# Optimization experiments

Hardware: AMD Instinct MI355X
Metric: run time of the kernel (lower is better)

## Reference

```python
import jax, jax.numpy as jnp
import numpy as np

N_EMBD = 768
N_HEAD = 12
BLOCK_SIZE = 1024


def setup_inputs() -> dict:
    key = jax.random.key(0)
    ks = jax.random.split(key, 11)
    s = lambda fan_in: 1.0 / np.sqrt(fan_in)
    x = jax.random.normal(ks[0], (8, 1024, N_EMBD), dtype=jnp.float32)
    return {
        "x": x,
        "ln1_g": jnp.ones((N_EMBD,), jnp.float32),
        "ln1_b": jnp.zeros((N_EMBD,), jnp.float32),
        "w_attn": jax.random.normal(ks[1], (N_EMBD, 3 * N_EMBD), jnp.float32) * s(N_EMBD),
        "b_attn": jnp.zeros((3 * N_EMBD,), jnp.float32),
        "w_proj": jax.random.normal(ks[2], (N_EMBD, N_EMBD), jnp.float32) * s(N_EMBD),
        "b_proj": jnp.zeros((N_EMBD,), jnp.float32),
        "ln2_g": jnp.ones((N_EMBD,), jnp.float32),
        "ln2_b": jnp.zeros((N_EMBD,), jnp.float32),
        "w_fc": jax.random.normal(ks[3], (N_EMBD, 4 * N_EMBD), jnp.float32) * s(N_EMBD),
        "b_fc": jnp.zeros((4 * N_EMBD,), jnp.float32),
        "w_fc_proj": jax.random.normal(ks[4], (4 * N_EMBD, N_EMBD), jnp.float32) * s(4 * N_EMBD),
        "b_fc_proj": jnp.zeros((N_EMBD,), jnp.float32),
    }


def _layernorm(x, g, b, eps=1e-5):
    mu = jnp.mean(x, axis=-1, keepdims=True)
    var = jnp.var(x, axis=-1, keepdims=True)
    return (x - mu) * jax.lax.rsqrt(var + eps) * g + b


def _gelu_tanh(x):
    # GELU with tanh approximation (matches nn.GELU(approximate='tanh'))
    c = np.sqrt(2.0 / np.pi).astype(np.float32)
    return 0.5 * x * (1.0 + jnp.tanh(c * (x + 0.044715 * x * x * x)))


def _attn(x, w_attn, b_attn, w_proj, b_proj):
    B, T, C = x.shape
    hs = C // N_HEAD
    qkv = x @ w_attn + b_attn  # [B,T,3C]
    q, k, v = jnp.split(qkv, 3, axis=-1)
    # [B,T,C] -> [B,nh,T,hs]
    to_heads = lambda t: t.reshape(B, T, N_HEAD, hs).transpose(0, 2, 1, 3)
    q, k, v = to_heads(q), to_heads(k), to_heads(v)
    att = jnp.einsum('bhqd,bhkd->bhqk', q, k) * (1.0 / np.sqrt(hs))
    causal = jnp.tril(jnp.ones((T, T), bool))
    att = jnp.where(causal, att, -jnp.inf)
    att = jax.nn.softmax(att, axis=-1)
    y = jnp.einsum('bhqk,bhkd->bhqd', att, v)  # [B,nh,T,hs]
    y = y.transpose(0, 2, 1, 3).reshape(B, T, C)
    return y @ w_proj + b_proj


def reference(x, ln1_g, ln1_b, w_attn, b_attn, w_proj, b_proj,
              ln2_g, ln2_b, w_fc, b_fc, w_fc_proj, b_fc_proj):
    x = x + _attn(_layernorm(x, ln1_g, ln1_b), w_attn, b_attn, w_proj, b_proj)
    h = _layernorm(x, ln2_g, ln2_b)
    h = _gelu_tanh(h @ w_fc + b_fc) @ w_fc_proj + b_fc_proj
    return x + h
```

## Files before the change

### kernel.cpp

```cpp
#include <hip/hip_runtime.h>

typedef __bf16 bf16x8 __attribute__((ext_vector_type(8)));
typedef float  f32x4  __attribute__((ext_vector_type(4)));
typedef unsigned short ushort8 __attribute__((ext_vector_type(8)));

__device__ __forceinline__ unsigned short f2bf(float f) {
    unsigned u = __float_as_uint(f);
    u += 0x7FFFu + ((u >> 16) & 1u);
    return (unsigned short)(u >> 16);
}

__device__ __forceinline__ f32x4 mfma16x16x32(bf16x8 a, bf16x8 b, f32x4 c) {
    return __builtin_amdgcn_mfma_f32_16x16x32_bf16(a, b, c, 0, 0, 0);
}

__device__ __forceinline__ bf16x8 ld8(const unsigned short* p) {
    return __builtin_bit_cast(bf16x8, *(const ushort8*)p);
}

__device__ __forceinline__ float exp2_fast(float x) {
    float r; asm("v_exp_f32 %0, %1" : "=v"(r) : "v"(x)); return r;
}

__device__ __forceinline__ void glds16(const unsigned short* g, unsigned short* l) {
    __builtin_amdgcn_global_load_lds(
        (const __attribute__((address_space(1))) void*)g,
        (__attribute__((address_space(3))) void*)l, 16, 0, 0);
}

__device__ __forceinline__ float gelu_tanh(float x) {
    const float c = 0.7978845608028654f;
    float z = c * (x + 0.044715f * x * x * x);
    float e = __expf(2.f * z);
    float th = 1.f - 2.f / (e + 1.f);
    return 0.5f * x * (1.f + th);
}

#define N_EMBD 768
#define SEQ    1024
#define NHEAD  12
#define HS     64
#define MROWS  8192

__global__ __launch_bounds__(256) void tcast_kernel(const float* __restrict__ in,
                                                    unsigned short* __restrict__ out,
                                                    int K, int N) {
    __shared__ float tile[32][33];
    int nb = blockIdx.x * 32, kb = blockIdx.y * 32;
    int tx = threadIdx.x, ty = threadIdx.y;
#pragma unroll
    for (int i = 0; i < 4; i++) {
        int k = kb + ty + i * 8;
        tile[ty + i * 8][tx] = in[(size_t)k * N + nb + tx];
    }
    __syncthreads();
#pragma unroll
    for (int i = 0; i < 4; i++) {
        int n = nb + ty + i * 8;
        out[(size_t)n * K + kb + tx] = f2bf(tile[tx][ty + i * 8]);
    }
}

__global__ __launch_bounds__(256) void ln_kernel(const float* __restrict__ x,
                                                 const float* __restrict__ g,
                                                 const float* __restrict__ b,
                                                 unsigned short* __restrict__ out) {
    const int row = blockIdx.x * 4 + (threadIdx.x >> 6);
    const int lane = threadIdx.x & 63;
    const float* xr = x + (size_t)row * N_EMBD;
    float v[12], s = 0.f, s2 = 0.f;
#pragma unroll
    for (int i = 0; i < 12; i++) {
        v[i] = xr[lane + i * 64];
        s += v[i]; s2 += v[i] * v[i];
    }
#pragma unroll
    for (int m = 1; m < 64; m <<= 1) { s += __shfl_xor(s, m); s2 += __shfl_xor(s2, m); }
    float mu  = s * (1.f / N_EMBD);
    float var = s2 * (1.f / N_EMBD) - mu * mu;
    float inv = rsqrtf(var + 1e-5f);
#pragma unroll
    for (int i = 0; i < 12; i++) {
        int c = lane + i * 64;
        out[(size_t)row * N_EMBD + c] = f2bf((v[i] - mu) * inv * g[c] + b[c]);
    }
}

template <int EPI, int WM>
__global__ __launch_bounds__(256) void gemm_bt_kernel(
    const unsigned short* __restrict__ A, const unsigned short* __restrict__ BT,
    const float* __restrict__ bias, const float* __restrict__ res,
    float* __restrict__ outF, unsigned short* __restrict__ outB,
    int M, int N, int K) {
    constexpr int BM = WM * 32;
    constexpr int ASZ = BM * 64;
    constexpr int BSZ = 128 * 64;
    __shared__ __attribute__((aligned(16))) unsigned short As[2 * ASZ];
    __shared__ __attribute__((aligned(16))) unsigned short Bs[2 * BSZ];
    const int gx = gridDim.x;
    const int slot = blockIdx.y * gx + blockIdx.x;
    const int chunk = (gx * gridDim.y) >> 3;
    const int logical = (slot & 7) * chunk + (slot >> 3);
    const int m0 = (logical / gx) * BM, n0 = (logical % gx) * 128;
    const int t = threadIdx.x, lane = t & 63, wid = t >> 6;
    const int wr = wid >> 1, wc = wid & 1;

    f32x4 acc[WM][4] = {};

    const int rrow = lane & 15, g = lane >> 4;
    const int swz8 = (rrow & 7) << 3;

    const int srow = t >> 3;
    const int scol = ((t & 7) ^ (srow & 7)) * 8;

    const int NT = K >> 6;

    const unsigned short* aP[WM];
    const unsigned short* bP[4];
#pragma unroll
    for (int i = 0; i < WM; i++) aP[i] = &A[(size_t)(m0 + i * 32 + srow) * K + scol];
#pragma unroll
    for (int i = 0; i < 4; i++)  bP[i] = &BT[(size_t)(n0 + i * 32 + srow) * K + scol];

    auto stage = [&](int buf) {
#pragma unroll
        for (int i = 0; i < WM; i++) {
            glds16(aP[i], &As[buf * ASZ + i * 2048 + wid * 512]);
            aP[i] += 64;
        }
#pragma unroll
        for (int i = 0; i < 4; i++) {
            glds16(bP[i], &Bs[buf * BSZ + i * 2048 + wid * 512]);
            bP[i] += 64;
        }
    };

    stage(0);
    __syncthreads();

    int cur = 0;
    for (int kt = 0; kt < NT; ++kt) {
        if (kt + 1 < NT) stage(cur ^ 1);
        const unsigned short* ab = &As[cur * ASZ];
        const unsigned short* bb = &Bs[cur * BSZ];
#pragma unroll
        for (int s = 0; s < 2; s++) {
            bf16x8 af[WM], bfr[4];
#pragma unroll
            for (int i = 0; i < WM; i++) {
                int row = wr * (WM * 16) + i * 16 + rrow;
                af[i] = ld8(&ab[row * 64 + ((((s << 2) | g) << 3) ^ swz8)]);
            }
#pragma unroll
            for (int j = 0; j < 4; j++) {
                int row = wc * 64 + j * 16 + rrow;
                bfr[j] = ld8(&bb[row * 64 + ((((s << 2) | g) << 3) ^ swz8)]);
            }
#pragma unroll
            for (int i = 0; i < WM; i++)
#pragma unroll
                for (int j = 0; j < 4; j++) acc[i][j] = mfma16x16x32(af[i], bfr[j], acc[i][j]);
        }
        __syncthreads();
        cur ^= 1;
    }

    const int crow = g * 4, ccol = rrow;
#pragma unroll
    for (int i = 0; i < WM; i++) {
        int gr0 = m0 + wr * (WM * 16) + i * 16 + crow;
#pragma unroll
        for (int j = 0; j < 4; j++) {
            int gc = n0 + wc * 64 + j * 16 + ccol;
            float bv = bias[gc];
#pragma unroll
            for (int r = 0; r < 4; r++) {
                int gr = gr0 + r;
                float v = acc[i][j][r] + bv;
                if constexpr (EPI == 1) v = gelu_tanh(v);
                if constexpr (EPI == 2) {
                    outF[(size_t)gr * N + gc] = v + res[(size_t)gr * N + gc];
                } else {
                    outB[(size_t)gr * N + gc] = f2bf(v);
                }
            }
        }
    }
}

#define SCALE_LOG2E 0.18033688011112042f

__global__ __launch_bounds__(256, 4) void attn_kernel(const unsigned short* __restrict__ qkv,
                                                      unsigned short* __restrict__ yb) {
    const int slot = blockIdx.y * 8 + blockIdx.x;
    const int logical = (slot & 7) * 96 + (slot >> 3);
    const int p = logical & 7;
    const int bh = logical >> 3;
    const int b = bh / NHEAD, h = bh % NHEAD;
    const int t = threadIdx.x, lane = t & 63, wid = t >> 6;
    const int q0A = p * 64 + wid * 16, q0B = (15 - p) * 64 + wid * 16;
    const int ntA = p + 1, ntB = 16 - p;
    const int rrow = lane & 15, g = lane >> 4, kg8 = g * 8;

    __shared__ __attribute__((aligned(16))) unsigned short Ks[64 * 64];
    __shared__ __attribute__((aligned(16))) unsigned short Vt[64 * 88];
    __shared__ __attribute__((aligned(16))) unsigned short Ps[4][2][16 * 80];

    bf16x8 qfA[2], qfB[2];
    {
        size_t baseA = ((size_t)(b * SEQ + q0A + rrow)) * 2304 + h * HS;
        qfA[0] = ld8(&qkv[baseA + kg8]);
        qfA[1] = ld8(&qkv[baseA + 32 + kg8]);
        size_t baseB = ((size_t)(b * SEQ + q0B + rrow)) * 2304 + h * HS;
        qfB[0] = ld8(&qkv[baseB + kg8]);
        qfB[1] = ld8(&qkv[baseB + 32 + kg8]);
    }

    f32x4 yA[4] = {}, yB[4] = {};
    float lA[4] = {0.f, 0.f, 0.f, 0.f}, lB[4] = {0.f, 0.f, 0.f, 0.f};

    const int kr0 = t >> 3, kr1 = kr0 + 32;
    const int kc0 = ((t & 7) ^ (kr0 & 7)) * 8;
    const int vd = t & 63, vk = (t >> 6) * 16;

    unsigned short* PB = &Ps[wid][0][0];
    unsigned short* PA = &Ps[wid][1][0];
    const bf16x8 vones = __builtin_bit_cast(bf16x8,
        (ushort8){0x3F80, 0x3F80, 0x3F80, 0x3F80, 0x3F80, 0x3F80, 0x3F80, 0x3F80});

    for (int tt = 0; tt < ntB; tt++) {
        const int kv0 = tt * 64;
        const bool doA = (tt < ntA);
        const bool maskB = (tt == ntB - 1), maskA = (tt == ntA - 1);
        __syncthreads();
        glds16(&qkv[((size_t)(b * SEQ + kv0 + kr0)) * 2304 + 768 + h * HS + kc0], &Ks[wid * 512]);
        glds16(&qkv[((size_t)(b * SEQ + kv0 + kr1)) * 2304 + 768 + h * HS + kc0], &Ks[2048 + wid * 512]);
        ushort8 vlo, vhi;
#pragma unroll
        for (int i = 0; i < 8; i++)
            vlo[i] = qkv[((size_t)(b * SEQ + kv0 + vk + i)) * 2304 + 1536 + h * HS + vd];
#pragma unroll
        for (int i = 0; i < 8; i++)
            vhi[i] = qkv[((size_t)(b * SEQ + kv0 + vk + 8 + i)) * 2304 + 1536 + h * HS + vd];
        *(ushort8*)&Vt[vd * 88 + vk] = vlo;
        *(ushort8*)&Vt[vd * 88 + vk + 8] = vhi;
        __syncthreads();

        f32x4 sB[4], sA[4];
#pragma unroll
        for (int ct = 0; ct < 4; ct++) {
            const int j = ct * 16 + rrow;
            const unsigned short* kr = &Ks[j * 64];
            bf16x8 k0 = ld8(&kr[((g    ) ^ (j & 7)) * 8]);
            bf16x8 k1 = ld8(&kr[((g + 4) ^ (j & 7)) * 8]);
            f32x4 zB = {};
            zB = mfma16x16x32(qfB[0], k0, zB);
            zB = mfma16x16x32(qfB[1], k1, zB);
            sB[ct] = zB;
            if (doA) {
                f32x4 zA = {};
                zA = mfma16x16x32(qfA[0], k0, zA);
                zA = mfma16x16x32(qfA[1], k1, zA);
                sA[ct] = zA;
            }
        }
        const int qrbB = q0B + g * 4, qrbA = q0A + g * 4;
#pragma unroll
        for (int ct = 0; ct < 4; ct++) {
            const int j = ct * 16 + rrow, jj = kv0 + j;
#pragma unroll
            for (int r = 0; r < 4; r++) {
                float v = sB[ct][r] * SCALE_LOG2E;
                if (maskB && jj > qrbB + r) v = -1e30f;
                const int q = g * 4 + r;
                PB[q * 80 + (j ^ ((q & 7) << 3))] = f2bf(exp2_fast(v));
            }
        }
        if (doA) {
#pragma unroll
            for (int ct = 0; ct < 4; ct++) {
                const int j = ct * 16 + rrow, jj = kv0 + j;
#pragma unroll
                for (int r = 0; r < 4; r++) {
                    float v = sA[ct][r] * SCALE_LOG2E;
                    if (maskA && jj > qrbA + r) v = -1e30f;
                    const int q = g * 4 + r;
                    PA[q * 80 + (j ^ ((q & 7) << 3))] = f2bf(exp2_fast(v));
                }
            }
        }
        asm volatile("s_waitcnt lgkmcnt(0)" ::: "memory");
        __builtin_amdgcn_sched_barrier(0);
        const int sw = (rrow & 7) << 3;
        bf16x8 paB0 = ld8(&PB[rrow * 80 + ((kg8     ) ^ sw)]);
        bf16x8 paB1 = ld8(&PB[rrow * 80 + ((kg8 + 32) ^ sw)]);
        bf16x8 paA0, paA1;
        if (doA) {
            paA0 = ld8(&PA[rrow * 80 + ((kg8     ) ^ sw)]);
            paA1 = ld8(&PA[rrow * 80 + ((kg8 + 32) ^ sw)]);
        }
        __builtin_amdgcn_s_setprio(1);
        f32x4 ssB = {};
        ssB = mfma16x16x32(paB0, vones, ssB);
        ssB = mfma16x16x32(paB1, vones, ssB);
#pragma unroll
        for (int r = 0; r < 4; r++) lB[r] += ssB[r];
        if (doA) {
            f32x4 ssA = {};
            ssA = mfma16x16x32(paA0, vones, ssA);
            ssA = mfma16x16x32(paA1, vones, ssA);
#pragma unroll
            for (int r = 0; r < 4; r++) lA[r] += ssA[r];
        }
#pragma unroll
        for (int dt = 0; dt < 4; dt++) {
            const unsigned short* vr = &Vt[(dt * 16 + rrow) * 88];
            bf16x8 v0 = ld8(&vr[kg8]);
            bf16x8 v1 = ld8(&vr[kg8 + 32]);
            yB[dt] = mfma16x16x32(paB0, v0, yB[dt]);
            yB[dt] = mfma16x16x32(paB1, v1, yB[dt]);
            if (doA) {
                yA[dt] = mfma16x16x32(paA0, v0, yA[dt]);
                yA[dt] = mfma16x16x32(paA1, v1, yA[dt]);
            }
        }
        __builtin_amdgcn_s_setprio(0);
    }

#pragma unroll
    for (int dt = 0; dt < 4; dt++)
#pragma unroll
        for (int r = 0; r < 4; r++) {
            int col = h * HS + dt * 16 + rrow;
            yb[((size_t)(b * SEQ + q0B + g * 4 + r)) * N_EMBD + col] = f2bf(yB[dt][r] / lB[r]);
            yb[((size_t)(b * SEQ + q0A + g * 4 + r)) * N_EMBD + col] = f2bf(yA[dt][r] / lA[r]);
        }
}

extern "C" void kernel_launch(void* const* d_in, const int* in_sizes, int n_in,
                              void* d_out, int out_size, void* d_ws, size_t ws_size,
                              hipStream_t stream) {
    const float* x        = (const float*)d_in[0];
    const float* ln1_g    = (const float*)d_in[1];
    const float* ln1_b    = (const float*)d_in[2];
    const float* w_attn   = (const float*)d_in[3];
    const float* b_attn   = (const float*)d_in[4];
    const float* w_proj   = (const float*)d_in[5];
    const float* b_proj   = (const float*)d_in[6];
    const float* ln2_g    = (const float*)d_in[7];
    const float* ln2_b    = (const float*)d_in[8];
    const float* w_fc     = (const float*)d_in[9];
    const float* b_fc     = (const float*)d_in[10];
    const float* w_fcp    = (const float*)d_in[11];
    const float* b_fcp    = (const float*)d_in[12];
    float* out = (float*)d_out;

    unsigned short* ws = (unsigned short*)d_ws;
    unsigned short* wT_attn = ws;
    unsigned short* wT_proj = wT_attn + 2304 * 768;
    unsigned short* wT_fc   = wT_proj + 768 * 768;
    unsigned short* wT_fcp  = wT_fc   + 3072 * 768;
    unsigned short* xb      = wT_fcp  + 768 * 3072;
    unsigned short* qkv     = xb      + (size_t)MROWS * 768;
    unsigned short* yb      = qkv     + (size_t)MROWS * 2304;
    unsigned short* act     = qkv;
    float* x2 = (float*)(yb + (size_t)MROWS * 768);

    dim3 tb(32, 8);
    tcast_kernel<<<dim3(2304 / 32, 768 / 32), tb, 0, stream>>>(w_attn, wT_attn, 768, 2304);
    tcast_kernel<<<dim3(768 / 32, 768 / 32),  tb, 0, stream>>>(w_proj, wT_proj, 768, 768);
    tcast_kernel<<<dim3(3072 / 32, 768 / 32), tb, 0, stream>>>(w_fc,   wT_fc,   768, 3072);
    tcast_kernel<<<dim3(768 / 32, 3072 / 32), tb, 0, stream>>>(w_fcp,  wT_fcp,  3072, 768);

    ln_kernel<<<MROWS / 4, 256, 0, stream>>>(x, ln1_g, ln1_b, xb);
    gemm_bt_kernel<0, 4><<<dim3(2304 / 128, MROWS / 128), 256, 0, stream>>>(
        xb, wT_attn, b_attn, nullptr, nullptr, qkv, MROWS, 2304, 768);
    attn_kernel<<<dim3(8, 96), 256, 0, stream>>>(qkv, yb);
    gemm_bt_kernel<2, 2><<<dim3(768 / 128, MROWS / 64), 256, 0, stream>>>(
        yb, wT_proj, b_proj, x, x2, nullptr, MROWS, 768, 768);
    ln_kernel<<<MROWS / 4, 256, 0, stream>>>(x2, ln2_g, ln2_b, xb);
    gemm_bt_kernel<1, 4><<<dim3(3072 / 128, MROWS / 128), 256, 0, stream>>>(
        xb, wT_fc, b_fc, nullptr, nullptr, act, MROWS, 3072, 768);
    gemm_bt_kernel<2, 2><<<dim3(768 / 128, MROWS / 64), 256, 0, stream>>>(
        act, wT_fcp, b_fcp, x2, out, nullptr, MROWS, 768, 3072);
}
```

Baseline: 253.2 us.

## Add two-wave 128x128 GEMM kernel with 64x128 per-wave tiles for large GEMMs

Adds a new GEMM kernel that runs two waves per block, each computing a 64x128 output sub-tile with a 4x8 accumulator array. The goal is more register-level reuse of A and B fragments per LDS read. It replaces the QKV, FC and FC-proj GEMMs; the FC-proj GEMM also moves from 64-row to 128-row tiles, which halves its grid. The cost is a much higher register count (128 accumulator floats per lane), lower occupancy, and fewer blocks for the N=768 GEMM.

```diff
diff --git a/kernel.cpp b/kernel.cpp
--- a/kernel.cpp
+++ b/kernel.cpp
@@ -83,6 +83,92 @@
     for (int i = 0; i < 12; i++) {
         int c = lane + i * 64;
         out[(size_t)row * N_EMBD + c] = f2bf((v[i] - mu) * inv * g[c] + b[c]);
+    }
+}
+
+template <int EPI>
+__global__ __launch_bounds__(128) void gemm_w2_kernel(
+    const unsigned short* __restrict__ A, const unsigned short* __restrict__ BT,
+    const float* __restrict__ bias, const float* __restrict__ res,
+    float* __restrict__ outF, unsigned short* __restrict__ outB,
+    int M, int N, int K) {
+    __shared__ __attribute__((aligned(16))) unsigned short As[2 * 8192];
+    __shared__ __attribute__((aligned(16))) unsigned short Bs[2 * 8192];
+    const int gx = gridDim.x;
+    const int slot = blockIdx.y * gx + blockIdx.x;
+    const int chunk = (gx * gridDim.y) >> 3;
+    const int logical = (slot & 7) * chunk + (slot >> 3);
+    const int m0 = (logical / gx) * 128, n0 = (logical % gx) * 128;
+    const int t = threadIdx.x, lane = t & 63, w = t >> 6;
+    const int rrow = lane & 15, g = lane >> 4;
+    const int swz8 = (rrow & 7) << 3;
+
+    f32x4 acc[4][8] = {};
+
+    const int srow = t >> 3;
+    const int scol = ((t & 7) ^ (srow & 7)) * 8;
+    const unsigned short* aP = &A[(size_t)(m0 + srow) * K + scol];
+    const unsigned short* bP = &BT[(size_t)(n0 + srow) * K + scol];
+    const int dbase = w * 512;
+
+    const int NT = K >> 6;
+
+    auto stage = [&](int buf) {
+#pragma unroll
+        for (int i = 0; i < 8; i++)
+            glds16(aP + (size_t)(i * 16) * K, &As[buf * 8192 + i * 1024 + dbase]);
+#pragma unroll
+        for (int i = 0; i < 8; i++)
+            glds16(bP + (size_t)(i * 16) * K, &Bs[buf * 8192 + i * 1024 + dbase]);
+        aP += 64; bP += 64;
+    };
+
+    stage(0);
+    __syncthreads();
+
+    int cur = 0;
+    for (int kt = 0; kt < NT; ++kt) {
+        if (kt + 1 < NT) stage(cur ^ 1);
+        const unsigned short* ab = &As[cur * 8192];
+        const unsigned short* bb = &Bs[cur * 8192];
+#pragma unroll
+        for (int s = 0; s < 2; s++) {
+            const int ko = (((s << 2) | g) << 3) ^ swz8;
+            bf16x8 af[4];
+#pragma unroll
+            for (int i = 0; i < 4; i++)
+                af[i] = ld8(&ab[(w * 64 + i * 16 + rrow) * 64 + ko]);
+#pragma unroll
+            for (int j = 0; j < 8; j++) {
+                bf16x8 bf = ld8(&bb[(j * 16 + rrow) * 64 + ko]);
+#pragma unroll
+                for (int i = 0; i < 4; i++)
+                    acc[i][j] = mfma16x16x32(af[i], bf, acc[i][j]);
+            }
+        }
+        __syncthreads();
+        cur ^= 1;
+    }
+
+#pragma unroll
+    for (int i = 0; i < 4; i++) {
+        int gr0 = m0 + w * 64 + i * 16 + g * 4;
+#pragma unroll
+        for (int j = 0; j < 8; j++) {
+            int gc = n0 + j * 16 + rrow;
+            float bv = bias[gc];
+#pragma unroll
+            for (int r = 0; r < 4; r++) {
+                int gr = gr0 + r;
+                float v = acc[i][j][r] + bv;
+                if constexpr (EPI == 1) v = gelu_tanh(v);
+                if constexpr (EPI == 2) {
+                    outF[(size_t)gr * N + gc] = v + res[(size_t)gr * N + gc];
+                } else {
+                    outB[(size_t)gr * N + gc] = f2bf(v);
+                }
+            }
+        }
     }
 }
 
@@ -373,14 +459,14 @@
     tcast_kernel<<<dim3(768 / 32, 3072 / 32), tb, 0, stream>>>(w_fcp,  wT_fcp,  3072, 768);
 
     ln_kernel<<<MROWS / 4, 256, 0, stream>>>(x, ln1_g, ln1_b, xb);
-    gemm_bt_kernel<0, 4><<<dim3(2304 / 128, MROWS / 128), 256, 0, stream>>>(
+    gemm_w2_kernel<0><<<dim3(2304 / 128, MROWS / 128), 128, 0, stream>>>(
         xb, wT_attn, b_attn, nullptr, nullptr, qkv, MROWS, 2304, 768);
     attn_kernel<<<dim3(8, 96), 256, 0, stream>>>(qkv, yb);
     gemm_bt_kernel<2, 2><<<dim3(768 / 128, MROWS / 64), 256, 0, stream>>>(
         yb, wT_proj, b_proj, x, x2, nullptr, MROWS, 768, 768);
     ln_kernel<<<MROWS / 4, 256, 0, stream>>>(x2, ln2_g, ln2_b, xb);
-    gemm_bt_kernel<1, 4><<<dim3(3072 / 128, MROWS / 128), 256, 0, stream>>>(
+    gemm_w2_kernel<1><<<dim3(3072 / 128, MROWS / 128), 128, 0, stream>>>(
         xb, wT_fc, b_fc, nullptr, nullptr, act, MROWS, 3072, 768);
-    gemm_bt_kernel<2, 2><<<dim3(768 / 128, MROWS / 64), 256, 0, stream>>>(
+    gemm_w2_kernel<2><<<dim3(768 / 128, MROWS / 128), 128, 0, stream>>>(
         act, wT_fcp, b_fcp, x2, out, nullptr, MROWS, 768, 3072);
 }
```

New measurement: 302.6 us. 1.19x slower.

## Load 128-key KV tiles per barrier pair and share one P buffer

Applied to the files above, without the earlier changes.

The attention kernel now stages 128 keys of K and V into shared memory per iteration and processes them as two 64-key sub-steps, which halves the number of __syncthreads round trips per KV sweep. The B and A query groups are handled one after the other through a single per-wave P scratch buffer instead of two, with occupancy dropped from 4 to 3 blocks per SM to fit the larger LDS footprint. The costs are lower occupancy, serialised A/B softmax phases, and some wasted loading when ntB is odd.

```diff
diff --git a/kernel.cpp b/kernel.cpp
--- a/kernel.cpp
+++ b/kernel.cpp
@@ -190,7 +190,7 @@
 
 #define SCALE_LOG2E 0.18033688011112042f
 
-__global__ __launch_bounds__(256, 4) void attn_kernel(const unsigned short* __restrict__ qkv,
+__global__ __launch_bounds__(256, 3) void attn_kernel(const unsigned short* __restrict__ qkv,
                                                       unsigned short* __restrict__ yb) {
     const int slot = blockIdx.y * 8 + blockIdx.x;
     const int logical = (slot & 7) * 96 + (slot >> 3);
@@ -200,11 +200,12 @@
     const int t = threadIdx.x, lane = t & 63, wid = t >> 6;
     const int q0A = p * 64 + wid * 16, q0B = (15 - p) * 64 + wid * 16;
     const int ntA = p + 1, ntB = 16 - p;
+    const int ntT = (ntB + 1) >> 1;
     const int rrow = lane & 15, g = lane >> 4, kg8 = g * 8;
 
-    __shared__ __attribute__((aligned(16))) unsigned short Ks[64 * 64];
-    __shared__ __attribute__((aligned(16))) unsigned short Vt[64 * 88];
-    __shared__ __attribute__((aligned(16))) unsigned short Ps[4][2][16 * 80];
+    __shared__ __attribute__((aligned(16))) unsigned short Ks[128 * 64];
+    __shared__ __attribute__((aligned(16))) unsigned short Vt[64 * 152];
+    __shared__ __attribute__((aligned(16))) unsigned short Ps[4][16 * 80];
 
     bf16x8 qfA[2], qfB[2];
     {
@@ -219,112 +220,123 @@
     f32x4 yA[4] = {}, yB[4] = {};
     float lA[4] = {0.f, 0.f, 0.f, 0.f}, lB[4] = {0.f, 0.f, 0.f, 0.f};
 
-    const int kr0 = t >> 3, kr1 = kr0 + 32;
-    const int kc0 = ((t & 7) ^ (kr0 & 7)) * 8;
-    const int vd = t & 63, vk = (t >> 6) * 16;
-
-    unsigned short* PB = &Ps[wid][0][0];
-    unsigned short* PA = &Ps[wid][1][0];
+    const int kr = t >> 3;
+    const int kc = ((t & 7) ^ (kr & 7)) * 8;
+    const int vd = t & 63, vk = (t >> 6) * 32;
+
+    unsigned short* P = &Ps[wid][0];
     const bf16x8 vones = __builtin_bit_cast(bf16x8,
         (ushort8){0x3F80, 0x3F80, 0x3F80, 0x3F80, 0x3F80, 0x3F80, 0x3F80, 0x3F80});
-
-    for (int tt = 0; tt < ntB; tt++) {
-        const int kv0 = tt * 64;
-        const bool doA = (tt < ntA);
-        const bool maskB = (tt == ntB - 1), maskA = (tt == ntA - 1);
+    const int sw = (rrow & 7) << 3;
+
+    for (int tt = 0; tt < ntT; tt++) {
+        const int kv0 = tt * 128;
         __syncthreads();
-        glds16(&qkv[((size_t)(b * SEQ + kv0 + kr0)) * 2304 + 768 + h * HS + kc0], &Ks[wid * 512]);
-        glds16(&qkv[((size_t)(b * SEQ + kv0 + kr1)) * 2304 + 768 + h * HS + kc0], &Ks[2048 + wid * 512]);
-        ushort8 vlo, vhi;
-#pragma unroll
-        for (int i = 0; i < 8; i++)
-            vlo[i] = qkv[((size_t)(b * SEQ + kv0 + vk + i)) * 2304 + 1536 + h * HS + vd];
-#pragma unroll
-        for (int i = 0; i < 8; i++)
-            vhi[i] = qkv[((size_t)(b * SEQ + kv0 + vk + 8 + i)) * 2304 + 1536 + h * HS + vd];
-        *(ushort8*)&Vt[vd * 88 + vk] = vlo;
-        *(ushort8*)&Vt[vd * 88 + vk + 8] = vhi;
+#pragma unroll
+        for (int i = 0; i < 4; i++)
+            glds16(&qkv[((size_t)(b * SEQ + kv0 + i * 32 + kr)) * 2304 + 768 + h * HS + kc],
+                   &Ks[i * 2048 + wid * 512]);
+#pragma unroll
+        for (int iv = 0; iv < 4; iv++) {
+            ushort8 v8;
+#pragma unroll
+            for (int i = 0; i < 8; i++)
+                v8[i] = qkv[((size_t)(b * SEQ + kv0 + vk + iv * 8 + i)) * 2304 + 1536 + h * HS + vd];
+            *(ushort8*)&Vt[vd * 152 + vk + iv * 8] = v8;
+        }
         __syncthreads();
 
-        f32x4 sB[4], sA[4];
-#pragma unroll
-        for (int ct = 0; ct < 4; ct++) {
-            const int j = ct * 16 + rrow;
-            const unsigned short* kr = &Ks[j * 64];
-            bf16x8 k0 = ld8(&kr[((g    ) ^ (j & 7)) * 8]);
-            bf16x8 k1 = ld8(&kr[((g + 4) ^ (j & 7)) * 8]);
-            f32x4 zB = {};
-            zB = mfma16x16x32(qfB[0], k0, zB);
-            zB = mfma16x16x32(qfB[1], k1, zB);
-            sB[ct] = zB;
+#pragma unroll
+        for (int hh = 0; hh < 2; hh++) {
+            const int sidx = tt * 2 + hh;
+            if (sidx >= ntB) continue;
+            const bool doA = (sidx < ntA);
+            const bool maskB = (sidx == ntB - 1), maskA = (sidx == ntA - 1);
+            const int kvs = kv0 + hh * 64;
+
+            f32x4 sB[4], sA[4];
+#pragma unroll
+            for (int ct = 0; ct < 4; ct++) {
+                const int j = ct * 16 + rrow;
+                const unsigned short* krow = &Ks[(hh * 64 + j) * 64];
+                bf16x8 k0 = ld8(&krow[((g    ) ^ (j & 7)) * 8]);
+                bf16x8 k1 = ld8(&krow[((g + 4) ^ (j & 7)) * 8]);
+                f32x4 zB = {};
+                zB = mfma16x16x32(qfB[0], k0, zB);
+                zB = mfma16x16x32(qfB[1], k1, zB);
+                sB[ct] = zB;
+                if (doA) {
+                    f32x4 zA = {};
+                    zA = mfma16x16x32(qfA[0], k0, zA);
+                    zA = mfma16x16x32(qfA[1], k1, zA);
+                    sA[ct] = zA;
+                }
+            }
+
+            const int qrbB = q0B + g * 4;
+#pragma unroll
+            for (int ct = 0; ct < 4; ct++) {
+                const int j = ct * 16 + rrow, jj = kvs + j;
+#pragma unroll
+                for (int r = 0; r < 4; r++) {
+                    float v = sB[ct][r] * SCALE_LOG2E;
+                    if (maskB && jj > qrbB + r) v = -1e30f;
+                    const int q = g * 4 + r;
+                    P[q * 80 + (j ^ ((q & 7) << 3))] = f2bf(exp2_fast(v));
+                }
+            }
+            asm volatile("s_waitcnt lgkmcnt(0)" ::: "memory");
+            __builtin_amdgcn_sched_barrier(0);
+            {
+                bf16x8 pa0 = ld8(&P[rrow * 80 + ((kg8     ) ^ sw)]);
+                bf16x8 pa1 = ld8(&P[rrow * 80 + ((kg8 + 32) ^ sw)]);
+                __builtin_amdgcn_s_setprio(1);
+                f32x4 ss = {};
+                ss = mfma16x16x32(pa0, vones, ss);
+                ss = mfma16x16x32(pa1, vones, ss);
+#pragma unroll
+                for (int r = 0; r < 4; r++) lB[r] += ss[r];
+#pragma unroll
+                for (int dt = 0; dt < 4; dt++) {
+                    const unsigned short* vr = &Vt[(dt * 16 + rrow) * 152 + hh * 64];
+                    yB[dt] = mfma16x16x32(pa0, ld8(&vr[kg8     ]), yB[dt]);
+                    yB[dt] = mfma16x16x32(pa1, ld8(&vr[kg8 + 32]), yB[dt]);
+                }
+                __builtin_amdgcn_s_setprio(0);
+            }
+
             if (doA) {
-                f32x4 zA = {};
-                zA = mfma16x16x32(qfA[0], k0, zA);
-                zA = mfma16x16x32(qfA[1], k1, zA);
-                sA[ct] = zA;
-            }
-        }
-        const int qrbB = q0B + g * 4, qrbA = q0A + g * 4;
-#pragma unroll
-        for (int ct = 0; ct < 4; ct++) {
-            const int j = ct * 16 + rrow, jj = kv0 + j;
-#pragma unroll
-            for (int r = 0; r < 4; r++) {
-                float v = sB[ct][r] * SCALE_LOG2E;
-                if (maskB && jj > qrbB + r) v = -1e30f;
-                const int q = g * 4 + r;
-                PB[q * 80 + (j ^ ((q & 7) << 3))] = f2bf(exp2_fast(v));
-            }
-        }
-        if (doA) {
-#pragma unroll
-            for (int ct = 0; ct < 4; ct++) {
-                const int j = ct * 16 + rrow, jj = kv0 + j;
-#pragma unroll
-                for (int r = 0; r < 4; r++) {
-                    float v = sA[ct][r] * SCALE_LOG2E;
-                    if (maskA && jj > qrbA + r) v = -1e30f;
-                    const int q = g * 4 + r;
-                    PA[q * 80 + (j ^ ((q & 7) << 3))] = f2bf(exp2_fast(v));
-                }
-            }
-        }
-        asm volatile("s_waitcnt lgkmcnt(0)" ::: "memory");
-        __builtin_amdgcn_sched_barrier(0);
-        const int sw = (rrow & 7) << 3;
-        bf16x8 paB0 = ld8(&PB[rrow * 80 + ((kg8     ) ^ sw)]);
-        bf16x8 paB1 = ld8(&PB[rrow * 80 + ((kg8 + 32) ^ sw)]);
-        bf16x8 paA0, paA1;
-        if (doA) {
-            paA0 = ld8(&PA[rrow * 80 + ((kg8     ) ^ sw)]);
-            paA1 = ld8(&PA[rrow * 80 + ((kg8 + 32) ^ sw)]);
-        }
-        __builtin_amdgcn_s_setprio(1);
-        f32x4 ssB = {};
-        ssB = mfma16x16x32(paB0, vones, ssB);
-        ssB = mfma16x16x32(paB1, vones, ssB);
-#pragma unroll
-        for (int r = 0; r < 4; r++) lB[r] += ssB[r];
-        if (doA) {
-            f32x4 ssA = {};
-            ssA = mfma16x16x32(paA0, vones, ssA);
-            ssA = mfma16x16x32(paA1, vones, ssA);
-#pragma unroll
-            for (int r = 0; r < 4; r++) lA[r] += ssA[r];
-        }
-#pragma unroll
-        for (int dt = 0; dt < 4; dt++) {
-            const unsigned short* vr = &Vt[(dt * 16 + rrow) * 88];
-            bf16x8 v0 = ld8(&vr[kg8]);
-            bf16x8 v1 = ld8(&vr[kg8 + 32]);
-            yB[dt] = mfma16x16x32(paB0, v0, yB[dt]);
-            yB[dt] = mfma16x16x32(paB1, v1, yB[dt]);
-            if (doA) {
-                yA[dt] = mfma16x16x32(paA0, v0, yA[dt]);
-                yA[dt] = mfma16x16x32(paA1, v1, yA[dt]);
-            }
-        }
-        __builtin_amdgcn_s_setprio(0);
+                const int qrbA = q0A + g * 4;
+#pragma unroll
+                for (int ct = 0; ct < 4; ct++) {
+                    const int j = ct * 16 + rrow, jj = kvs + j;
+#pragma unroll
+                    for (int r = 0; r < 4; r++) {
+                        float v = sA[ct][r] * SCALE_LOG2E;
+                        if (maskA && jj > qrbA + r) v = -1e30f;
+                        const int q = g * 4 + r;
+                        P[q * 80 + (j ^ ((q & 7) << 3))] = f2bf(exp2_fast(v));
+                    }
+                }
+                asm volatile("s_waitcnt lgkmcnt(0)" ::: "memory");
+                __builtin_amdgcn_sched_barrier(0);
+                bf16x8 pa0 = ld8(&P[rrow * 80 + ((kg8     ) ^ sw)]);
+                bf16x8 pa1 = ld8(&P[rrow * 80 + ((kg8 + 32) ^ sw)]);
+                __builtin_amdgcn_s_setprio(1);
+                f32x4 ss = {};
+                ss = mfma16x16x32(pa0, vones, ss);
+                ss = mfma16x16x32(pa1, vones, ss);
+#pragma unroll
+                for (int r = 0; r < 4; r++) lA[r] += ss[r];
+#pragma unroll
+                for (int dt = 0; dt < 4; dt++) {
+                    const unsigned short* vr = &Vt[(dt * 16 + rrow) * 152 + hh * 64];
+                    yA[dt] = mfma16x16x32(pa0, ld8(&vr[kg8     ]), yA[dt]);
+                    yA[dt] = mfma16x16x32(pa1, ld8(&vr[kg8 + 32]), yA[dt]);
+                }
+                __builtin_amdgcn_s_setprio(0);
+            }
+        }
     }
 
 #pragma unroll
```

Result: faster. 242.5 us, median of 3 (-4.2%).
